# Kernel tuning notes

Measured on AMD Instinct MI355X. Metric: run time of the kernel, lower is better.

## Reference

```python
import jax, jax.numpy as jnp
import numpy as np

N = 50000
IN_DIM, HID_DIM, OUT_DIM = 512, 256, 64
E = 800000


def setup_inputs() -> dict:
    key = jax.random.key(0)
    k1, k2, k3, k4, k5, k6 = jax.random.split(key, 6)
    x = jax.random.normal(k1, (N, IN_DIM), dtype=jnp.float32)
    edge_index = jax.random.randint(k2, (2, E), 0, N, dtype=jnp.int64)
    # GCNConv parameters (glorot-ish scale)
    W1 = jax.random.normal(k3, (IN_DIM, HID_DIM), dtype=jnp.float32) * (1.0 / np.sqrt(IN_DIM))
    b1 = jnp.zeros((HID_DIM,), dtype=jnp.float32)
    W2 = jax.random.normal(k4, (HID_DIM, OUT_DIM), dtype=jnp.float32) * (1.0 / np.sqrt(HID_DIM))
    b2 = jnp.zeros((OUT_DIM,), dtype=jnp.float32)
    return {"x": x, "W1": W1, "b1": b1, "W2": W2, "b2": b2, "edge_index": edge_index}


def _gcn_conv(x, W, b, src, dst, norm, n_nodes):
    # PyG GCNConv: out[dst] = sum_e norm_e * (x @ W)[src_e] + b
    h = x @ W                              # [N, out]
    msg = h[src] * norm[:, None]           # [E+N, out] gather + scale
    out = jax.ops.segment_sum(msg, dst, num_segments=n_nodes)  # scatter-add
    return out + b


def reference(x, W1, b1, W2, b2, edge_index):
    n = x.shape[0]
    # add self-loops (PyG default add_self_loops=True)
    loop = jnp.arange(n, dtype=edge_index.dtype)
    src = jnp.concatenate([edge_index[0], loop])
    dst = jnp.concatenate([edge_index[1], loop])
    # symmetric normalization: deg computed on destination (in-degree incl. self-loop)
    deg = jax.ops.segment_sum(jnp.ones_like(dst, dtype=x.dtype), dst, num_segments=n)
    dis = jnp.where(deg > 0, jax.lax.rsqrt(jnp.maximum(deg, 1.0)), 0.0)
    norm = dis[src] * dis[dst]
    h = _gcn_conv(x, W1, b1, src, dst, norm, n)
    h = jax.nn.relu(h)
    out = _gcn_conv(h, W2, b2, src, dst, norm, n)
    return out
```

## Files before the change

### kernel.cpp

```cpp
#include <hip/hip_runtime.h>
#include <hip/hip_bf16.h>
#include <hip/hip_fp16.h>
#include <stdint.h>

typedef _Float16 half8_t __attribute__((ext_vector_type(8)));
typedef float f32x4_t __attribute__((ext_vector_type(4)));

#define LBAR() do { asm volatile("s_waitcnt lgkmcnt(0)" ::: "memory"); \
                    __builtin_amdgcn_s_barrier(); } while (0)


__global__ __launch_bounds__(256) void detect_i64_kernel(const int* __restrict__ idx,
                                                         int* __restrict__ flag,
                                                         int* __restrict__ bcnt) {
    int t = threadIdx.x;
    if (t < 64) {
        int v = idx[2 * t + 1];
        unsigned long long b = __ballot(v == 0);
        if (t == 0) *flag = (b == 0xFFFFFFFFFFFFFFFFULL) ? 1 : 0;
    }
    bcnt[t] = 0;
}

__device__ __forceinline__ int load_idx(const int* __restrict__ idx, long long pos, int is64) {
    return is64 ? idx[2 * pos] : idx[pos];
}

#define EPB 4096

__global__ __launch_bounds__(256) void bin_count_kernel(
        const int* __restrict__ idx, const int* __restrict__ flag,
        int* __restrict__ bcnt, int E, int N) {
    __shared__ int hist[256];
    hist[threadIdx.x] = 0;
    __syncthreads();
    const int is64 = *flag;
    const int base = blockIdx.x * EPB;
    const int cnt = (E - base < EPB) ? E - base : EPB;
    for (int i = threadIdx.x; i < cnt; i += 256) {
        int d = load_idx(idx, (long long)E + base + i, is64);
        if ((unsigned)d < (unsigned)N) atomicAdd(&hist[d >> 8], 1);
    }
    __syncthreads();
    int h = hist[threadIdx.x];
    if (h) atomicAdd(&bcnt[threadIdx.x], h);
}

__global__ __launch_bounds__(256) void scan_buckets_kernel(
        const int* __restrict__ bcnt, int* __restrict__ bbase,
        int* __restrict__ bcur, int NB) {
    __shared__ int buf[256];
    int t = threadIdx.x;
    int v = (t < NB) ? bcnt[t] : 0;
    buf[t] = v;
    __syncthreads();
    #pragma unroll
    for (int off = 1; off < 256; off <<= 1) {
        int u = (t >= off) ? buf[t - off] : 0;
        __syncthreads();
        buf[t] += u;
        __syncthreads();
    }
    int excl = buf[t] - v;
    if (t < NB) { bbase[t] = excl; bcur[t] = excl; }
    if (t == NB - 1) bbase[NB] = buf[t];
}

__global__ __launch_bounds__(256) void bin_scatter_kernel(
        const int* __restrict__ idx, const int* __restrict__ flag,
        int* __restrict__ bcur, unsigned* __restrict__ packed, int E, int N) {
    __shared__ int cur[256];
    cur[threadIdx.x] = 0;
    __syncthreads();
    const int is64 = *flag;
    const int base = blockIdx.x * EPB;
    const int cnt = (E - base < EPB) ? E - base : EPB;
    for (int i = threadIdx.x; i < cnt; i += 256) {
        int d = load_idx(idx, (long long)E + base + i, is64);
        if ((unsigned)d < (unsigned)N) atomicAdd(&cur[d >> 8], 1);
    }
    __syncthreads();
    int h = cur[threadIdx.x];
    int bs = h ? atomicAdd(&bcur[threadIdx.x], h) : 0;
    __syncthreads();
    cur[threadIdx.x] = bs;
    __syncthreads();
    for (int i = threadIdx.x; i < cnt; i += 256) {
        int d = load_idx(idx, (long long)E + base + i, is64);
        if ((unsigned)d >= (unsigned)N) continue;
        int s = load_idx(idx, base + i, is64);
        if ((unsigned)s >= (unsigned)N) s = 0;
        int pos = atomicAdd(&cur[d >> 8], 1);
        packed[pos] = (unsigned)s | ((unsigned)(d & 255) << 16);
    }
}

__global__ __launch_bounds__(256) void bucket_sort_kernel(
        const unsigned* __restrict__ packed, const int* __restrict__ bbase,
        int* __restrict__ csr_src, int* __restrict__ offsets,
        float* __restrict__ dis, int N, int NB) {
    __shared__ int buf[256];
    __shared__ int cur[256];
    const int b = blockIdx.x;
    const int t = threadIdx.x;
    cur[t] = 0;
    __syncthreads();
    const int e0 = bbase[b], e1 = bbase[b + 1];
    for (int i = e0 + t; i < e1; i += 256)
        atomicAdd(&cur[(packed[i] >> 16) & 255], 1);
    __syncthreads();
    int v = cur[t];
    buf[t] = v;
    __syncthreads();
    #pragma unroll
    for (int off = 1; off < 256; off <<= 1) {
        int u = (t >= off) ? buf[t - off] : 0;
        __syncthreads();
        buf[t] += u;
        __syncthreads();
    }
    int excl = buf[t] - v;
    cur[t] = excl;
    int node = b * 256 + t;
    if (node < N) {
        offsets[node] = e0 + excl;
        dis[node] = rsqrtf((float)(v + 1));
    }
    if (b == NB - 1 && t == 0) offsets[N] = bbase[NB];
    __syncthreads();
    for (int i = e0 + t; i < e1; i += 256) {
        unsigned rec = packed[i];
        int dl = (rec >> 16) & 255;
        int pos = atomicAdd(&cur[dl], 1);
        csr_src[e0 + pos] = (int)(rec & 0xFFFF);
    }
}

__global__ void wt_kernel(const float* __restrict__ W1, const float* __restrict__ W2,
                          _Float16* __restrict__ w1t, _Float16* __restrict__ w2t) {
    int p = blockIdx.x * 256 + threadIdx.x;
    if (p < 512 * 256) {
        int k = p >> 8, n = p & 255;
        w1t[n * 512 + k] = (_Float16)W1[p];
    } else {
        int q = p - 512 * 256;
        if (q < 256 * 64) {
            int k = q >> 6, n = q & 63;
            w2t[n * 256 + k] = (_Float16)W2[q];
        }
    }
}

__global__ __launch_bounds__(256, 3) void gemm1_kernel(
        const float* __restrict__ x, const _Float16* __restrict__ w1t,
        const float* __restrict__ dis, _Float16* __restrict__ h1s, int M) {
    __shared__ _Float16 As[4 * 65 * 8];
    __shared__ _Float16 Bs[4 * 257 * 8];
    const int tid = threadIdx.x;
    const int brow = blockIdx.x * 64;
    const int w = tid >> 6, lane = tid & 63;
    const int wcol = w * 64;
    const int lrow = lane & 15, lkb = lane >> 4;

    const int arow = tid >> 2, akb = tid & 3;
    const int gr = brow + arow;
    const bool aval = gr < M;
    const float* xptr = x + (size_t)(aval ? gr : 0) * 512 + akb * 8;
    const _Float16* bbase = w1t + (size_t)arow * 512 + akb * 8;
    const int awr = (akb * 65 + arow) << 3;
    const int bwr0 = (akb * 257 + arow) << 3;

    f32x4_t acc[4][4];
    #pragma unroll
    for (int mi = 0; mi < 4; ++mi)
        #pragma unroll
        for (int nj = 0; nj < 4; ++nj) acc[mi][nj] = (f32x4_t)0.f;

    float4 au = make_float4(0.f, 0.f, 0.f, 0.f);
    float4 av = make_float4(0.f, 0.f, 0.f, 0.f);
    half8_t bh0, bh1, bh2, bh3;

    if (aval) { au = *(const float4*)(xptr); av = *(const float4*)(xptr + 4); }
    bh0 = *(const half8_t*)(bbase);
    bh1 = *(const half8_t*)(bbase + 64 * 512);
    bh2 = *(const half8_t*)(bbase + 128 * 512);
    bh3 = *(const half8_t*)(bbase + 192 * 512);

    for (int t = 0; t < 16; ++t) {
        LBAR();
        half8_t ha;
        ha[0] = (_Float16)au.x; ha[1] = (_Float16)au.y;
        ha[2] = (_Float16)au.z; ha[3] = (_Float16)au.w;
        ha[4] = (_Float16)av.x; ha[5] = (_Float16)av.y;
        ha[6] = (_Float16)av.z; ha[7] = (_Float16)av.w;
        *(half8_t*)&As[awr] = ha;
        *(half8_t*)&Bs[bwr0] = bh0;
        *(half8_t*)&Bs[bwr0 + 64 * 8] = bh1;
        *(half8_t*)&Bs[bwr0 + 128 * 8] = bh2;
        *(half8_t*)&Bs[bwr0 + 192 * 8] = bh3;
        LBAR();
        if (t < 15) {
            int k0 = (t + 1) * 32;
            if (aval) {
                au = *(const float4*)(xptr + k0);
                av = *(const float4*)(xptr + k0 + 4);
            }
            bh0 = *(const half8_t*)(bbase + k0);
            bh1 = *(const half8_t*)(bbase + k0 + 64 * 512);
            bh2 = *(const half8_t*)(bbase + k0 + 128 * 512);
            bh3 = *(const half8_t*)(bbase + k0 + 192 * 512);
        }
        half8_t a[4], b[4];
        #pragma unroll
        for (int mi = 0; mi < 4; ++mi)
            a[mi] = *(const half8_t*)&As[(lkb * 65 + mi * 16 + lrow) << 3];
        #pragma unroll
        for (int nj = 0; nj < 4; ++nj)
            b[nj] = *(const half8_t*)&Bs[(lkb * 257 + wcol + nj * 16 + lrow) << 3];
        #pragma unroll
        for (int mi = 0; mi < 4; ++mi)
            #pragma unroll
            for (int nj = 0; nj < 4; ++nj)
                acc[mi][nj] = __builtin_amdgcn_mfma_f32_16x16x32_f16(a[mi], b[nj], acc[mi][nj], 0, 0, 0);
    }
    #pragma unroll
    for (int mi = 0; mi < 4; ++mi) {
        #pragma unroll
        for (int r = 0; r < 4; ++r) {
            int grow = brow + mi * 16 + (lane >> 4) * 4 + r;
            if (grow >= M) continue;
            float s = dis[grow];
            #pragma unroll
            for (int nj = 0; nj < 4; ++nj) {
                int col = wcol + nj * 16 + lrow;
                h1s[((size_t)(col >> 5) * M + grow) * 32 + (col & 31)] =
                    (_Float16)(acc[mi][nj][r] * s);
            }
        }
    }
}

__global__ __launch_bounds__(256, 4) void gemm2_kernel(
        const _Float16* __restrict__ a1s, const _Float16* __restrict__ w2t,
        const float* __restrict__ dis, _Float16* __restrict__ h2s, int M) {
    __shared__ _Float16 As[4 * 65 * 8];
    __shared__ _Float16 Bs[4 * 65 * 8];
    const int tid = threadIdx.x;
    const int brow = blockIdx.x * 64;
    const int w = tid >> 6, lane = tid & 63;
    const int lrow = lane & 15, lkb = lane >> 4;

    const int arow = tid >> 2, akb = tid & 3;
    const int gr = brow + arow;
    const bool aval = gr < M;
    const _Float16* aptr = a1s + ((size_t)(aval ? gr : 0)) * 32 + akb * 8;
    const _Float16* bptr = w2t + (size_t)arow * 256 + akb * 8;
    const int awr = (akb * 65 + arow) << 3;

    f32x4_t acc[4];
    #pragma unroll
    for (int nj = 0; nj < 4; ++nj) acc[nj] = (f32x4_t)0.f;

    const half8_t zero8 = (half8_t)(_Float16)0.f;
    half8_t ah = zero8, bh;
    if (aval) ah = *(const half8_t*)(aptr);
    bh = *(const half8_t*)(bptr);

    for (int t = 0; t < 8; ++t) {
        LBAR();
        *(half8_t*)&As[awr] = ah;
        *(half8_t*)&Bs[awr] = bh;
        LBAR();
        if (t < 7) {
            if (aval) ah = *(const half8_t*)(aptr + (size_t)(t + 1) * M * 32);
            bh = *(const half8_t*)(bptr + (t + 1) * 32);
        }
        half8_t a = *(const half8_t*)&As[(lkb * 65 + w * 16 + lrow) << 3];
        half8_t b[4];
        #pragma unroll
        for (int nj = 0; nj < 4; ++nj)
            b[nj] = *(const half8_t*)&Bs[(lkb * 65 + nj * 16 + lrow) << 3];
        #pragma unroll
        for (int nj = 0; nj < 4; ++nj)
            acc[nj] = __builtin_amdgcn_mfma_f32_16x16x32_f16(a, b[nj], acc[nj], 0, 0, 0);
    }
    #pragma unroll
    for (int r = 0; r < 4; ++r) {
        int grow = brow + w * 16 + (lane >> 4) * 4 + r;
        if (grow >= M) continue;
        float s = dis[grow];
        #pragma unroll
        for (int nj = 0; nj < 4; ++nj) {
            int col = nj * 16 + lrow;
            h2s[((size_t)(col >> 5) * M + grow) * 32 + (col & 31)] =
                (_Float16)(acc[nj][r] * s);
        }
    }
}

__device__ __forceinline__ float4 up4(uint2 v) {
    __half2 h0 = *reinterpret_cast<__half2*>(&v.x);
    __half2 h1 = *reinterpret_cast<__half2*>(&v.y);
    float2 a = __half22float2(h0), b = __half22float2(h1);
    return make_float4(a.x, a.y, b.x, b.y);
}

__device__ __forceinline__ unsigned pkw(unsigned a, unsigned b) {
    __half2 ha = *reinterpret_cast<__half2*>(&a);
    __half2 hb = *reinterpret_cast<__half2*>(&b);
    __half2 r = __hadd2(ha, hb);
    return *reinterpret_cast<unsigned*>(&r);
}

__device__ __forceinline__ uint4 pk4(uint4 a, uint4 b) {
    uint4 r;
    r.x = pkw(a.x, b.x);
    r.y = pkw(a.y, b.y);
    r.z = pkw(a.z, b.z);
    r.w = pkw(a.w, b.w);
    return r;
}

template<int NCH, int FP16OUT>
__global__ __launch_bounds__(256) void aggv_kernel(
        const _Float16* __restrict__ g, const int* __restrict__ offsets,
        const int* __restrict__ csr_src, const float* __restrict__ dis,
        const float* __restrict__ bias, void* __restrict__ out, int N) {
    constexpr int CAP = 2048;
    __shared__ int lds_csr[CAP];
    const int chunk = blockIdx.x % NCH;
    const int nodeBase = (blockIdx.x / NCH) * 64;
    const int grp = threadIdx.x >> 2;
    const int cl = threadIdx.x & 3;
    const int node = nodeBase + grp;
    const bool active = node < N;
    const int nend = (nodeBase + 64 < N) ? nodeBase + 64 : N;
    const int blk0 = offsets[nodeBase];
    const int blk1 = offsets[nend];
    const uint4* gc = (const uint4*)g + (size_t)chunk * N * 4;

    int gs0 = 0, gs1 = 0;
    float s = 0.f;
    if (active) { gs0 = offsets[node]; gs1 = offsets[node + 1]; s = dis[node]; }

    float4 accLo = make_float4(0.f, 0.f, 0.f, 0.f);
    float4 accHi = make_float4(0.f, 0.f, 0.f, 0.f);
    if (active) {
        uint4 sv = gc[(size_t)node * 4 + cl];
        float4 lo = up4(make_uint2(sv.x, sv.y));
        float4 hi = up4(make_uint2(sv.z, sv.w));
        accLo.x += lo.x; accLo.y += lo.y; accLo.z += lo.z; accLo.w += lo.w;
        accHi.x += hi.x; accHi.y += hi.y; accHi.z += hi.z; accHi.w += hi.w;
    }

    for (int base = blk0; base < blk1; base += CAP) {
        const int cnt = (blk1 - base < CAP) ? blk1 - base : CAP;
        __syncthreads();
        for (int i = threadIdx.x; i < cnt; i += 256)
            lds_csr[i] = csr_src[base + i];
        __syncthreads();
        int lo_e = (gs0 > base ? gs0 : base) - base;
        int hi_e = (gs1 < base + cnt ? gs1 : base + cnt) - base;
        int e = lo_e;
        for (; e + 4 <= hi_e; e += 4) {
            int s0 = lds_csr[e], s1 = lds_csr[e + 1];
            int s2 = lds_csr[e + 2], s3 = lds_csr[e + 3];
            uint4 v0 = gc[(size_t)s0 * 4 + cl];
            uint4 v1 = gc[(size_t)s1 * 4 + cl];
            uint4 v2 = gc[(size_t)s2 * 4 + cl];
            uint4 v3 = gc[(size_t)s3 * 4 + cl];
            uint4 q = pk4(pk4(v0, v1), pk4(v2, v3));
            float4 flo = up4(make_uint2(q.x, q.y));
            float4 fhi = up4(make_uint2(q.z, q.w));
            accLo.x += flo.x; accLo.y += flo.y; accLo.z += flo.z; accLo.w += flo.w;
            accHi.x += fhi.x; accHi.y += fhi.y; accHi.z += fhi.z; accHi.w += fhi.w;
        }
        for (; e < hi_e; ++e) {
            int s0 = lds_csr[e];
            uint4 v = gc[(size_t)s0 * 4 + cl];
            float4 flo = up4(make_uint2(v.x, v.y));
            float4 fhi = up4(make_uint2(v.z, v.w));
            accLo.x += flo.x; accLo.y += flo.y; accLo.z += flo.z; accLo.w += flo.w;
            accHi.x += fhi.x; accHi.y += fhi.y; accHi.z += fhi.z; accHi.w += fhi.w;
        }
    }
    if (active) {
        float4 bb0 = *(const float4*)&bias[chunk * 32 + cl * 8];
        float4 bb1 = *(const float4*)&bias[chunk * 32 + cl * 8 + 4];
        float4 o0, o1;
        o0.x = fmaf(s, accLo.x, bb0.x);
        o0.y = fmaf(s, accLo.y, bb0.y);
        o0.z = fmaf(s, accLo.z, bb0.z);
        o0.w = fmaf(s, accLo.w, bb0.w);
        o1.x = fmaf(s, accHi.x, bb1.x);
        o1.y = fmaf(s, accHi.y, bb1.y);
        o1.z = fmaf(s, accHi.z, bb1.z);
        o1.w = fmaf(s, accHi.w, bb1.w);
        if (FP16OUT) {
            o0.x = fmaxf(o0.x, 0.f); o0.y = fmaxf(o0.y, 0.f);
            o0.z = fmaxf(o0.z, 0.f); o0.w = fmaxf(o0.w, 0.f);
            o1.x = fmaxf(o1.x, 0.f); o1.y = fmaxf(o1.y, 0.f);
            o1.z = fmaxf(o1.z, 0.f); o1.w = fmaxf(o1.w, 0.f);
            __half2 p0 = __float22half2_rn(make_float2(o0.x, o0.y));
            __half2 p1 = __float22half2_rn(make_float2(o0.z, o0.w));
            __half2 p2 = __float22half2_rn(make_float2(o1.x, o1.y));
            __half2 p3 = __float22half2_rn(make_float2(o1.z, o1.w));
            uint4 pv;
            pv.x = *reinterpret_cast<unsigned*>(&p0);
            pv.y = *reinterpret_cast<unsigned*>(&p1);
            pv.z = *reinterpret_cast<unsigned*>(&p2);
            pv.w = *reinterpret_cast<unsigned*>(&p3);
            ((uint4*)out)[((size_t)chunk * N + node) * 4 + cl] = pv;
        } else {
            ((float4*)out)[(size_t)node * (NCH * 8) + chunk * 8 + cl * 2]     = o0;
            ((float4*)out)[(size_t)node * (NCH * 8) + chunk * 8 + cl * 2 + 1] = o1;
        }
    }
}

extern "C" void kernel_launch(void* const* d_in, const int* in_sizes, int n_in,
                              void* d_out, int out_size, void* d_ws, size_t ws_size,
                              hipStream_t stream) {
    const float* x  = (const float*)d_in[0];
    const float* W1 = (const float*)d_in[1];
    const float* b1 = (const float*)d_in[2];
    const float* W2 = (const float*)d_in[3];
    const float* b2 = (const float*)d_in[4];
    const int* eidx = (const int*)d_in[5];

    const int HID = in_sizes[2];
    const int OUT = in_sizes[4];
    const int IN  = in_sizes[1] / HID;
    const int N   = in_sizes[0] / IN;
    const int E   = in_sizes[5] / 2;
    const int NB  = (N + 255) >> 8;

    char* ws = (char*)d_ws;
    size_t off = 0;
    auto alloc = [&](size_t bytes) {
        off = (off + 255) & ~(size_t)255;
        char* p = ws + off;
        off += bytes;
        return p;
    };
    float* dis       = (float*)alloc((size_t)N * 4);
    int* flag        = (int*)alloc(256);
    int* bcnt        = (int*)alloc(256 * 4);
    int* bbase       = (int*)alloc(260 * 4);
    int* bcur        = (int*)alloc(256 * 4);
    int* offsets     = (int*)alloc((size_t)(N + 1) * 4);
    unsigned* packed = (unsigned*)alloc((size_t)E * 4);
    int* csr_src     = (int*)alloc((size_t)E * 4);
    _Float16* w1t    = (_Float16*)alloc((size_t)IN * HID * 2);
    _Float16* w2t    = (_Float16*)alloc((size_t)HID * OUT * 2);
    _Float16* h1s    = (_Float16*)alloc((size_t)N * HID * 2);
    _Float16* a1s    = (_Float16*)alloc((size_t)N * HID * 2);
    _Float16* h2s    = (_Float16*)alloc((size_t)N * OUT * 2);

    const int nblkE = (E + EPB - 1) / EPB;

    detect_i64_kernel<<<1, 256, 0, stream>>>(eidx, flag, bcnt);
    bin_count_kernel<<<nblkE, 256, 0, stream>>>(eidx, flag, bcnt, E, N);
    scan_buckets_kernel<<<1, 256, 0, stream>>>(bcnt, bbase, bcur, NB);
    bin_scatter_kernel<<<nblkE, 256, 0, stream>>>(eidx, flag, bcur, packed, E, N);
    bucket_sort_kernel<<<NB, 256, 0, stream>>>(packed, bbase, csr_src, offsets, dis, N, NB);
    wt_kernel<<<(IN * HID + HID * OUT + 255) / 256, 256, 0, stream>>>(W1, W2, w1t, w2t);

    gemm1_kernel<<<(N + 63) / 64, 256, 0, stream>>>(x, w1t, dis, h1s, N);
    aggv_kernel<8, 1><<<((N + 63) / 64) * 8, 256, 0, stream>>>(h1s, offsets, csr_src, dis,
                                                               b1, a1s, N);
    gemm2_kernel<<<(N + 63) / 64, 256, 0, stream>>>(a1s, w2t, dis, h2s, N);
    aggv_kernel<2, 0><<<((N + 63) / 64) * 2, 256, 0, stream>>>(h2s, offsets, csr_src, dis,
                                                               b2, d_out, N);
}
```

Before: 149.5 us.

## Drop LDS staging in both GEMMs and load MFMA fragments directly from global

Both dense GEMM kernels stop staging A and B tiles through shared memory with barriers. Each lane now loads its MFMA fragments straight from global memory (converting x from fp32 to fp16 in registers) and relies on L1/L2 for reuse across waves. This removes LDS traffic and barrier synchronisation, but each wave re-reads the shared A rows and issues more, less coalesced global loads. Occupancy for gemm1 is lowered to 2 blocks per SM in launch bounds.

```diff
diff --git a/kernel.cpp b/kernel.cpp
--- a/kernel.cpp
+++ b/kernel.cpp
@@ -5,9 +5,6 @@
 
 typedef _Float16 half8_t __attribute__((ext_vector_type(8)));
 typedef float f32x4_t __attribute__((ext_vector_type(4)));
-
-#define LBAR() do { asm volatile("s_waitcnt lgkmcnt(0)" ::: "memory"); \
-                    __builtin_amdgcn_s_barrier(); } while (0)
 
 
 __global__ __launch_bounds__(256) void detect_i64_kernel(const int* __restrict__ idx,
@@ -151,24 +148,23 @@
     }
 }
 
-__global__ __launch_bounds__(256, 3) void gemm1_kernel(
+__global__ __launch_bounds__(256, 2) void gemm1_kernel(
         const float* __restrict__ x, const _Float16* __restrict__ w1t,
         const float* __restrict__ dis, _Float16* __restrict__ h1s, int M) {
-    __shared__ _Float16 As[4 * 65 * 8];
-    __shared__ _Float16 Bs[4 * 257 * 8];
     const int tid = threadIdx.x;
     const int brow = blockIdx.x * 64;
     const int w = tid >> 6, lane = tid & 63;
     const int wcol = w * 64;
     const int lrow = lane & 15, lkb = lane >> 4;
 
-    const int arow = tid >> 2, akb = tid & 3;
-    const int gr = brow + arow;
-    const bool aval = gr < M;
-    const float* xptr = x + (size_t)(aval ? gr : 0) * 512 + akb * 8;
-    const _Float16* bbase = w1t + (size_t)arow * 512 + akb * 8;
-    const int awr = (akb * 65 + arow) << 3;
-    const int bwr0 = (akb * 257 + arow) << 3;
+    const float* xp[4];
+    #pragma unroll
+    for (int mi = 0; mi < 4; ++mi) {
+        int r = brow + mi * 16 + lrow;
+        if (r >= M) r = M - 1;
+        xp[mi] = x + (size_t)r * 512 + lkb * 8;
+    }
+    const _Float16* wb = w1t + (size_t)(wcol + lrow) * 512 + lkb * 8;
 
     f32x4_t acc[4][4];
     #pragma unroll
@@ -176,47 +172,21 @@
         #pragma unroll
         for (int nj = 0; nj < 4; ++nj) acc[mi][nj] = (f32x4_t)0.f;
 
-    float4 au = make_float4(0.f, 0.f, 0.f, 0.f);
-    float4 av = make_float4(0.f, 0.f, 0.f, 0.f);
-    half8_t bh0, bh1, bh2, bh3;
-
-    if (aval) { au = *(const float4*)(xptr); av = *(const float4*)(xptr + 4); }
-    bh0 = *(const half8_t*)(bbase);
-    bh1 = *(const half8_t*)(bbase + 64 * 512);
-    bh2 = *(const half8_t*)(bbase + 128 * 512);
-    bh3 = *(const half8_t*)(bbase + 192 * 512);
-
-    for (int t = 0; t < 16; ++t) {
-        LBAR();
-        half8_t ha;
-        ha[0] = (_Float16)au.x; ha[1] = (_Float16)au.y;
-        ha[2] = (_Float16)au.z; ha[3] = (_Float16)au.w;
-        ha[4] = (_Float16)av.x; ha[5] = (_Float16)av.y;
-        ha[6] = (_Float16)av.z; ha[7] = (_Float16)av.w;
-        *(half8_t*)&As[awr] = ha;
-        *(half8_t*)&Bs[bwr0] = bh0;
-        *(half8_t*)&Bs[bwr0 + 64 * 8] = bh1;
-        *(half8_t*)&Bs[bwr0 + 128 * 8] = bh2;
-        *(half8_t*)&Bs[bwr0 + 192 * 8] = bh3;
-        LBAR();
-        if (t < 15) {
-            int k0 = (t + 1) * 32;
-            if (aval) {
-                au = *(const float4*)(xptr + k0);
-                av = *(const float4*)(xptr + k0 + 4);
-            }
-            bh0 = *(const half8_t*)(bbase + k0);
-            bh1 = *(const half8_t*)(bbase + k0 + 64 * 512);
-            bh2 = *(const half8_t*)(bbase + k0 + 128 * 512);
-            bh3 = *(const half8_t*)(bbase + k0 + 192 * 512);
-        }
+    #pragma unroll 2
+    for (int k0 = 0; k0 < 512; k0 += 32) {
         half8_t a[4], b[4];
         #pragma unroll
-        for (int mi = 0; mi < 4; ++mi)
-            a[mi] = *(const half8_t*)&As[(lkb * 65 + mi * 16 + lrow) << 3];
+        for (int mi = 0; mi < 4; ++mi) {
+            float4 u = *(const float4*)(xp[mi] + k0);
+            float4 v = *(const float4*)(xp[mi] + k0 + 4);
+            a[mi][0] = (_Float16)u.x; a[mi][1] = (_Float16)u.y;
+            a[mi][2] = (_Float16)u.z; a[mi][3] = (_Float16)u.w;
+            a[mi][4] = (_Float16)v.x; a[mi][5] = (_Float16)v.y;
+            a[mi][6] = (_Float16)v.z; a[mi][7] = (_Float16)v.w;
+        }
         #pragma unroll
         for (int nj = 0; nj < 4; ++nj)
-            b[nj] = *(const half8_t*)&Bs[(lkb * 257 + wcol + nj * 16 + lrow) << 3];
+            b[nj] = *(const half8_t*)(wb + (size_t)nj * 16 * 512 + k0);
         #pragma unroll
         for (int mi = 0; mi < 4; ++mi)
             #pragma unroll
@@ -243,57 +213,41 @@
 __global__ __launch_bounds__(256, 4) void gemm2_kernel(
         const _Float16* __restrict__ a1s, const _Float16* __restrict__ w2t,
         const float* __restrict__ dis, _Float16* __restrict__ h2s, int M) {
-    __shared__ _Float16 As[4 * 65 * 8];
-    __shared__ _Float16 Bs[4 * 65 * 8];
     const int tid = threadIdx.x;
     const int brow = blockIdx.x * 64;
     const int w = tid >> 6, lane = tid & 63;
     const int lrow = lane & 15, lkb = lane >> 4;
 
-    const int arow = tid >> 2, akb = tid & 3;
-    const int gr = brow + arow;
-    const bool aval = gr < M;
-    const _Float16* aptr = a1s + ((size_t)(aval ? gr : 0)) * 32 + akb * 8;
-    const _Float16* bptr = w2t + (size_t)arow * 256 + akb * 8;
-    const int awr = (akb * 65 + arow) << 3;
+    int r = brow + w * 16 + lrow;
+    if (r >= M) r = M - 1;
+    const _Float16* ap = a1s + (size_t)r * 32 + lkb * 8;
+    const _Float16* wp = w2t + (size_t)lrow * 256 + lkb * 8;
 
     f32x4_t acc[4];
     #pragma unroll
     for (int nj = 0; nj < 4; ++nj) acc[nj] = (f32x4_t)0.f;
 
-    const half8_t zero8 = (half8_t)(_Float16)0.f;
-    half8_t ah = zero8, bh;
-    if (aval) ah = *(const half8_t*)(aptr);
-    bh = *(const half8_t*)(bptr);
-
+    #pragma unroll 2
     for (int t = 0; t < 8; ++t) {
-        LBAR();
-        *(half8_t*)&As[awr] = ah;
-        *(half8_t*)&Bs[awr] = bh;
-        LBAR();
-        if (t < 7) {
-            if (aval) ah = *(const half8_t*)(aptr + (size_t)(t + 1) * M * 32);
-            bh = *(const half8_t*)(bptr + (t + 1) * 32);
-        }
-        half8_t a = *(const half8_t*)&As[(lkb * 65 + w * 16 + lrow) << 3];
+        half8_t a = *(const half8_t*)(ap + (size_t)t * M * 32);
         half8_t b[4];
         #pragma unroll
         for (int nj = 0; nj < 4; ++nj)
-            b[nj] = *(const half8_t*)&Bs[(lkb * 65 + nj * 16 + lrow) << 3];
+            b[nj] = *(const half8_t*)(wp + nj * 16 * 256 + t * 32);
         #pragma unroll
         for (int nj = 0; nj < 4; ++nj)
             acc[nj] = __builtin_amdgcn_mfma_f32_16x16x32_f16(a, b[nj], acc[nj], 0, 0, 0);
     }
     #pragma unroll
-    for (int r = 0; r < 4; ++r) {
-        int grow = brow + w * 16 + (lane >> 4) * 4 + r;
+    for (int rr = 0; rr < 4; ++rr) {
+        int grow = brow + w * 16 + (lane >> 4) * 4 + rr;
         if (grow >= M) continue;
         float s = dis[grow];
         #pragma unroll
         for (int nj = 0; nj < 4; ++nj) {
             int col = nj * 16 + lrow;
             h2s[((size_t)(col >> 5) * M + grow) * 32 + (col & 31)] =
-                (_Float16)(acc[nj][r] * s);
+                (_Float16)(acc[nj][rr] * s);
         }
     }
 }
```

After: 219.9 us. +47.1%, slower.

## Load W1 tiles directly into double-buffered LDS and raise gemm1 occupancy

Applied to the files above, without the earlier changes.

In gemm1, the W1 tile now goes straight from global memory into LDS with global_load_lds, into two LDS buffers alternating by k-step. This removes the register staging and the ds_write of B, and lets the next tile stream in while the current one is consumed. Out-of-range rows are clamped to the last row instead of branching. Launch bounds rise to 4 blocks per CU, which costs more LDS per block and tighter register limits. Correctness relies on the implicit vmcnt wait for the x loads also covering the async LDS writes before the second barrier.

```diff
diff --git a/kernel.cpp b/kernel.cpp
--- a/kernel.cpp
+++ b/kernel.cpp
@@ -8,6 +8,9 @@
 
 #define LBAR() do { asm volatile("s_waitcnt lgkmcnt(0)" ::: "memory"); \
                     __builtin_amdgcn_s_barrier(); } while (0)
+
+#define AS1(p) ((const __attribute__((address_space(1))) void*)(p))
+#define AS3(p) ((__attribute__((address_space(3))) void*)(p))
 
 
 __global__ __launch_bounds__(256) void detect_i64_kernel(const int* __restrict__ idx,
@@ -151,11 +154,11 @@
     }
 }
 
-__global__ __launch_bounds__(256, 3) void gemm1_kernel(
+__global__ __launch_bounds__(256, 4) void gemm1_kernel(
         const float* __restrict__ x, const _Float16* __restrict__ w1t,
         const float* __restrict__ dis, _Float16* __restrict__ h1s, int M) {
     __shared__ _Float16 As[4 * 65 * 8];
-    __shared__ _Float16 Bs[4 * 257 * 8];
+    __shared__ _Float16 Bs[2][4 * 257 * 8];
     const int tid = threadIdx.x;
     const int brow = blockIdx.x * 64;
     const int w = tid >> 6, lane = tid & 63;
@@ -163,12 +166,12 @@
     const int lrow = lane & 15, lkb = lane >> 4;
 
     const int arow = tid >> 2, akb = tid & 3;
-    const int gr = brow + arow;
-    const bool aval = gr < M;
-    const float* xptr = x + (size_t)(aval ? gr : 0) * 512 + akb * 8;
-    const _Float16* bbase = w1t + (size_t)arow * 512 + akb * 8;
+    int grc = brow + arow;
+    if (grc >= M) grc = M - 1;
+    const float* xptr = x + (size_t)grc * 512 + akb * 8;
     const int awr = (akb * 65 + arow) << 3;
-    const int bwr0 = (akb * 257 + arow) << 3;
+
+    const _Float16* bsrc = w1t + (size_t)(wcol + lane) * 512;
 
     f32x4_t acc[4][4];
     #pragma unroll
@@ -176,15 +179,13 @@
         #pragma unroll
         for (int nj = 0; nj < 4; ++nj) acc[mi][nj] = (f32x4_t)0.f;
 
-    float4 au = make_float4(0.f, 0.f, 0.f, 0.f);
-    float4 av = make_float4(0.f, 0.f, 0.f, 0.f);
-    half8_t bh0, bh1, bh2, bh3;
-
-    if (aval) { au = *(const float4*)(xptr); av = *(const float4*)(xptr + 4); }
-    bh0 = *(const half8_t*)(bbase);
-    bh1 = *(const half8_t*)(bbase + 64 * 512);
-    bh2 = *(const half8_t*)(bbase + 128 * 512);
-    bh3 = *(const half8_t*)(bbase + 192 * 512);
+    #pragma unroll
+    for (int i = 0; i < 4; ++i)
+        __builtin_amdgcn_global_load_lds(AS1(bsrc + i * 8),
+                                         AS3(&Bs[0][(i * 257 + wcol) << 3]),
+                                         16, 0, 0);
+    float4 au = *(const float4*)(xptr);
+    float4 av = *(const float4*)(xptr + 4);
 
     for (int t = 0; t < 16; ++t) {
         LBAR();
@@ -194,21 +195,16 @@
         ha[4] = (_Float16)av.x; ha[5] = (_Float16)av.y;
         ha[6] = (_Float16)av.z; ha[7] = (_Float16)av.w;
         *(half8_t*)&As[awr] = ha;
-        *(half8_t*)&Bs[bwr0] = bh0;
-        *(half8_t*)&Bs[bwr0 + 64 * 8] = bh1;
-        *(half8_t*)&Bs[bwr0 + 128 * 8] = bh2;
-        *(half8_t*)&Bs[bwr0 + 192 * 8] = bh3;
         LBAR();
         if (t < 15) {
             int k0 = (t + 1) * 32;
-            if (aval) {
-                au = *(const float4*)(xptr + k0);
-                av = *(const float4*)(xptr + k0 + 4);
-            }
-            bh0 = *(const half8_t*)(bbase + k0);
-            bh1 = *(const half8_t*)(bbase + k0 + 64 * 512);
-            bh2 = *(const half8_t*)(bbase + k0 + 128 * 512);
-            bh3 = *(const half8_t*)(bbase + k0 + 192 * 512);
+            #pragma unroll
+            for (int i = 0; i < 4; ++i)
+                __builtin_amdgcn_global_load_lds(AS1(bsrc + k0 + i * 8),
+                                                 AS3(&Bs[(t + 1) & 1][(i * 257 + wcol) << 3]),
+                                                 16, 0, 0);
+            au = *(const float4*)(xptr + k0);
+            av = *(const float4*)(xptr + k0 + 4);
         }
         half8_t a[4], b[4];
         #pragma unroll
@@ -216,7 +212,7 @@
             a[mi] = *(const half8_t*)&As[(lkb * 65 + mi * 16 + lrow) << 3];
         #pragma unroll
         for (int nj = 0; nj < 4; ++nj)
-            b[nj] = *(const half8_t*)&Bs[(lkb * 257 + wcol + nj * 16 + lrow) << 3];
+            b[nj] = *(const half8_t*)&Bs[t & 1][(lkb * 257 + wcol + nj * 16 + lrow) << 3];
         #pragma unroll
         for (int mi = 0; mi < 4; ++mi)
             #pragma unroll
```

After: 173.6 us. 1.16x slower.
